# Kernel optimization log

Measured on AMD Instinct MI355X. Metric: run time of the kernel, lower is better.

Reference implementation:

```python
import jax, jax.numpy as jnp
import numpy as np

INPUT_DIM = 1024
HIDDEN_DIM = 1024

def setup_inputs() -> dict:
    key = jax.random.key(0)
    ks = jax.random.split(key, 9)
    s_in = 1.0 / np.sqrt(INPUT_DIM)
    s_h = 1.0 / np.sqrt(HIDDEN_DIM)
    x = jax.random.normal(ks[0], (4, 2048, INPUT_DIM), dtype=jnp.float32)
    Wq = jax.random.uniform(ks[1], (INPUT_DIM, HIDDEN_DIM), jnp.float32, -s_in, s_in)
    bq = jax.random.uniform(ks[2], (HIDDEN_DIM,), jnp.float32, -s_in, s_in)
    Wk = jax.random.uniform(ks[3], (INPUT_DIM, HIDDEN_DIM), jnp.float32, -s_in, s_in)
    bk = jax.random.uniform(ks[4], (HIDDEN_DIM,), jnp.float32, -s_in, s_in)
    Wv = jax.random.uniform(ks[5], (INPUT_DIM, HIDDEN_DIM), jnp.float32, -s_in, s_in)
    bv = jax.random.uniform(ks[6], (HIDDEN_DIM,), jnp.float32, -s_in, s_in)
    Wo = jax.random.uniform(ks[7], (HIDDEN_DIM, INPUT_DIM), jnp.float32, -s_h, s_h)
    bo = jax.random.uniform(ks[8], (INPUT_DIM,), jnp.float32, -s_h, s_h)
    return {"x": x, "Wq": Wq, "bq": bq, "Wk": Wk, "bk": bk, "Wv": Wv, "bv": bv, "Wo": Wo, "bo": bo}

def reference(x, Wq, bq, Wk, bk, Wv, bv, Wo, bo):
    # x: [B, S, D_in]; scale uses x.shape[-1] (faithful to source, which divides by sqrt(input_dim))
    scale = 1.0 / jnp.sqrt(jnp.asarray(x.shape[-1], dtype=x.dtype))
    Q = jnp.einsum('bsd,dh->bsh', x, Wq) + bq
    K = jnp.einsum('bsd,dh->bsh', x, Wk) + bk
    V = jnp.einsum('bsd,dh->bsh', x, Wv) + bv
    scores = jnp.einsum('bqh,bkh->bqk', Q, K) * scale  # [B, S, S]
    attn = jax.nn.softmax(scores, axis=-1)
    ctx = jnp.einsum('bqk,bkh->bqh', attn, V)
    return jnp.einsum('bsh,hd->bsd', ctx, Wo) + bo
```

## Files before the change

### kernel.cpp

```cpp
#include <hip/hip_runtime.h>
#include <hip/hip_bf16.h>

typedef __attribute__((ext_vector_type(8))) short bf16x8;
typedef __attribute__((ext_vector_type(16))) float f32x16;
typedef __attribute__((ext_vector_type(4))) unsigned short us4;

#define AS1 __attribute__((address_space(1)))
#define AS3 __attribute__((address_space(3)))

__device__ __forceinline__ unsigned short f2bf(float f) {
  unsigned u = __float_as_uint(f);
  u += 0x7fff + ((u >> 16) & 1);
  return (unsigned short)(u >> 16);
}

__device__ __forceinline__ float bf2f(unsigned short h) {
  return __uint_as_float((unsigned)h << 16);
}

__device__ __forceinline__ void gload_lds16(const void* g, void* l) {
  __builtin_amdgcn_global_load_lds((const AS1 unsigned int*)g,
                                   (AS3 unsigned int*)l, 16, 0, 0);
}

template <typename OutT, bool BIAS, int MODE, int NJ>
__global__ __launch_bounds__(256, (NJ >= 3) ? 2 : 3) void gemm_bt(
    const unsigned short* __restrict__ A,
    const unsigned short* __restrict__ Bt,
    OutT* __restrict__ C,
    unsigned short* __restrict__ Vt,
    const float* __restrict__ bias,
    int Kd, int lda, int ldb, int ldc,
    long sA, long sB, long sC,
    float scale) {
  constexpr int BN    = NJ * 64;
  constexpr int ROWS  = 128 + BN;
  constexpr int SLOTS = ROWS / 16;
  __shared__ unsigned short lds[2][ROWS * 32];

  const int bz = blockIdx.z;
  A  += (size_t)bz * sA + (size_t)blockIdx.x * 128 * lda;
  Bt += (size_t)bz * sB + (size_t)blockIdx.y * BN * ldb;

  const int tid  = threadIdx.x;
  const int wave = tid >> 6;
  const int lane = tid & 63;
  const int wm   = (wave >> 1) * 64;
  const int wn   = (wave & 1) * (NJ * 32);
  const int l32  = lane & 31;
  const int half = lane >> 5;
  const int cg   = ((lane & 3) ^ ((lane >> 2) & 3) ^ (lane >> 4)) * 8;
  const int pswz = (l32 & 3) ^ ((l32 >> 2) & 3);

  auto stage = [&](int k0, int b) {
#pragma unroll
    for (int j = 0; j < SLOTS / 4; ++j) {
      const int s = wave + 4 * j;
      const int r = s * 16 + (lane >> 2);
      const unsigned short* src = (s < 8) ? (A + (size_t)r * lda)
                                          : (Bt + (size_t)(r - 128) * ldb);
      gload_lds16(src + k0 + cg, (char*)&lds[b][0] + s * 1024);
    }
  };

  f32x16 acc[2][NJ] = {};

  stage(0, 0);
  int cur = 0;
  for (int k0 = 0; k0 < Kd; k0 += 32) {
    __syncthreads();
    if (k0 + 32 < Kd) stage(k0 + 32, cur ^ 1);

    const unsigned short* base = &lds[cur][0];
    bf16x8 af[2][2], bfr[NJ][2];
#pragma unroll
    for (int t = 0; t < 2; ++t)
#pragma unroll
      for (int h = 0; h < 2; ++h) {
        const int p = ((2 * h + half) ^ pswz) * 8;
        af[t][h] = *(const bf16x8*)&base[(wm + t * 32 + l32) * 32 + p];
      }
#pragma unroll
    for (int u = 0; u < NJ; ++u)
#pragma unroll
      for (int h = 0; h < 2; ++h) {
        const int p = ((2 * h + half) ^ pswz) * 8;
        bfr[u][h] = *(const bf16x8*)&base[(128 + wn + u * 32 + l32) * 32 + p];
      }
#pragma unroll
    for (int t = 0; t < 2; ++t)
#pragma unroll
      for (int u = 0; u < NJ; ++u) {
        acc[t][u] = __builtin_amdgcn_mfma_f32_32x32x16_bf16(af[t][0], bfr[u][0], acc[t][u], 0, 0, 0);
        acc[t][u] = __builtin_amdgcn_mfma_f32_32x32x16_bf16(af[t][1], bfr[u][1], acc[t][u], 0, 0, 0);
      }
    cur ^= 1;
  }

  const int row0 = blockIdx.x * 128 + wm;
  const int colb = blockIdx.y * BN;

  if constexpr (MODE == 1) {
#pragma unroll
    for (int t = 0; t < 2; ++t) {
#pragma unroll
      for (int u = 0; u < NJ; ++u) {
        const int gcol  = colb + wn + u * 32;
        const int piece = gcol >> 10;
        const float bv  = BIAS ? bias[gcol + l32] : 0.0f;
        if (piece < 2) {
          OutT* dst = C + (size_t)piece * sC;
          const int col = (gcol & 1023) + l32;
#pragma unroll
          for (int r = 0; r < 16; ++r) {
            const int row = row0 + t * 32 + (r & 3) + 8 * (r >> 2) + 4 * half;
            dst[(size_t)row * ldc + col] = (OutT)f2bf(acc[t][u][r] * scale + bv);
          }
        } else {
          const int d = (gcol & 1023) + l32;
          const int b = row0 >> 11;
          const int sbase = (row0 & 2047) + t * 32 + 4 * half;
#pragma unroll
          for (int g = 0; g < 4; ++g) {
            const int s0 = sbase + 8 * g;
            us4 pk;
            pk.x = f2bf(acc[t][u][4 * g + 0] * scale + bv);
            pk.y = f2bf(acc[t][u][4 * g + 1] * scale + bv);
            pk.z = f2bf(acc[t][u][4 * g + 2] * scale + bv);
            pk.w = f2bf(acc[t][u][4 * g + 3] * scale + bv);
            *(us4*)&Vt[((size_t)b << 21) + (size_t)d * 2048 + s0] = pk;
          }
        }
      }
    }
  } else {
    C += (size_t)bz * sC;
    const int col0 = colb + wn;
#pragma unroll
    for (int t = 0; t < 2; ++t) {
#pragma unroll
      for (int u = 0; u < NJ; ++u) {
        const int col = col0 + u * 32 + l32;
        const float bv = BIAS ? bias[col0 + u * 32 + l32] : 0.0f;
#pragma unroll
        for (int r = 0; r < 16; ++r) {
          const int row = row0 + t * 32 + (r & 3) + 8 * (r >> 2) + 4 * half;
          const float v = acc[t][u][r] * scale + bv;
          if constexpr (sizeof(OutT) == 4)
            C[(size_t)row * ldc + col] = v;
          else
            C[(size_t)row * ldc + col] = (OutT)f2bf(v);
        }
      }
    }
  }
}

__global__ void cvt_x(const float* __restrict__ in, unsigned short* __restrict__ out, int n4) {
  const int i = blockIdx.x * blockDim.x + threadIdx.x;
  if (i < n4) {
    const float4 v = ((const float4*)in)[i];
    uint2 o;
    o.x = (unsigned)f2bf(v.x) | ((unsigned)f2bf(v.y) << 16);
    o.y = (unsigned)f2bf(v.z) | ((unsigned)f2bf(v.w) << 16);
    ((uint2*)out)[i] = o;
  }
}

__global__ void cvtT_w4(const float* __restrict__ Wq, const float* __restrict__ Wk,
                        const float* __restrict__ Wv, const float* __restrict__ Wo,
                        unsigned short* __restrict__ Wqkvb, unsigned short* __restrict__ Wob) {
  __shared__ unsigned short tile[64][65];
  const int z = blockIdx.z;
  const float* in = (z == 0) ? Wq : (z == 1) ? Wk : (z == 2) ? Wv : Wo;
  unsigned short* out = (z == 3) ? Wob : Wqkvb + (size_t)z * 1024 * 1024;
  const int r0 = blockIdx.y * 64, c0 = blockIdx.x * 64;
  for (int i = threadIdx.y; i < 64; i += 4)
    tile[i][threadIdx.x] = f2bf(in[(size_t)(r0 + i) * 1024 + c0 + threadIdx.x]);
  __syncthreads();
  for (int i = threadIdx.y; i < 64; i += 4)
    out[(size_t)(c0 + i) * 1024 + r0 + threadIdx.x] = tile[threadIdx.x][i];
}

__global__ void concat_bias(const float* __restrict__ bq, const float* __restrict__ bk,
                            const float* __restrict__ bv, float* __restrict__ dst) {
  const int z = blockIdx.x;
  const float* src = (z == 0) ? bq : (z == 1) ? bk : bv;
  const int i = threadIdx.x;
  ((float4*)(dst + z * 1024))[i] = ((const float4*)src)[i];
}

__global__ __launch_bounds__(256) void softmax_bf16(unsigned short* __restrict__ scores) {
  unsigned short* p = scores + (size_t)blockIdx.x * 2048;
  const int t = threadIdx.x;
  uint4 raw = ((const uint4*)p)[t];
  float v[8];
  v[0] = __uint_as_float(raw.x << 16); v[1] = __uint_as_float(raw.x & 0xffff0000u);
  v[2] = __uint_as_float(raw.y << 16); v[3] = __uint_as_float(raw.y & 0xffff0000u);
  v[4] = __uint_as_float(raw.z << 16); v[5] = __uint_as_float(raw.z & 0xffff0000u);
  v[6] = __uint_as_float(raw.w << 16); v[7] = __uint_as_float(raw.w & 0xffff0000u);

  float m = v[0];
#pragma unroll
  for (int i = 1; i < 8; ++i) m = fmaxf(m, v[i]);
#pragma unroll
  for (int off = 32; off; off >>= 1) m = fmaxf(m, __shfl_xor(m, off, 64));

  __shared__ float red[4];
  __shared__ float bcast[2];
  const int wave = t >> 6, lane = t & 63;
  if (lane == 0) red[wave] = m;
  __syncthreads();
  if (t == 0) bcast[0] = fmaxf(fmaxf(red[0], red[1]), fmaxf(red[2], red[3]));
  __syncthreads();
  m = bcast[0];

  float s = 0.f;
#pragma unroll
  for (int i = 0; i < 8; ++i) { v[i] = __expf(v[i] - m); s += v[i]; }
#pragma unroll
  for (int off = 32; off; off >>= 1) s += __shfl_xor(s, off, 64);
  if (lane == 0) red[wave] = s;
  __syncthreads();
  if (t == 0) bcast[1] = red[0] + red[1] + red[2] + red[3];
  __syncthreads();
  const float inv = 1.0f / bcast[1];

  uint4 ov;
  ov.x = (unsigned)f2bf(v[0] * inv) | ((unsigned)f2bf(v[1] * inv) << 16);
  ov.y = (unsigned)f2bf(v[2] * inv) | ((unsigned)f2bf(v[3] * inv) << 16);
  ov.z = (unsigned)f2bf(v[4] * inv) | ((unsigned)f2bf(v[5] * inv) << 16);
  ov.w = (unsigned)f2bf(v[6] * inv) | ((unsigned)f2bf(v[7] * inv) << 16);
  ((uint4*)p)[t] = ov;
}

extern "C" void kernel_launch(void* const* d_in, const int* in_sizes, int n_in,
                              void* d_out, int out_size, void* d_ws, size_t ws_size,
                              hipStream_t stream) {
  const float* x  = (const float*)d_in[0];
  const float* Wq = (const float*)d_in[1];
  const float* bq = (const float*)d_in[2];
  const float* Wk = (const float*)d_in[3];
  const float* bk = (const float*)d_in[4];
  const float* Wv = (const float*)d_in[5];
  const float* bv = (const float*)d_in[6];
  const float* Wo = (const float*)d_in[7];
  const float* bo = (const float*)d_in[8];
  float* out = (float*)d_out;

  char* ws = (char*)d_ws;
  size_t off = 0;
  auto alloc = [&](size_t bytes) { char* p = ws + off; off += (bytes + 255) & ~255UL; return p; };
  unsigned short* xb    = (unsigned short*)alloc(8192UL * 1024 * 2);
  unsigned short* Wqkvb = (unsigned short*)alloc(3072UL * 1024 * 2);
  unsigned short* Wob   = (unsigned short*)alloc(1024UL * 1024 * 2);
  float*          bqkv  = (float*)alloc(3072UL * 4);
  unsigned short* Qb    = (unsigned short*)alloc(8192UL * 1024 * 2);
  unsigned short* Kb    = (unsigned short*)alloc(8192UL * 1024 * 2);
  unsigned short* Vtb   = (unsigned short*)alloc(4UL * 1024 * 2048 * 2);
  unsigned short* attn  = (unsigned short*)alloc(8192UL * 2048 * 2);
  unsigned short* ctxb  = (unsigned short*)alloc(8192UL * 1024 * 2);

  const dim3 blk(256);

  cvt_x<<<2097152 / 256, 256, 0, stream>>>(x, xb, 2097152);
  cvtT_w4<<<dim3(16, 16, 4), dim3(64, 4), 0, stream>>>(Wq, Wk, Wv, Wo, Wqkvb, Wob);
  concat_bias<<<3, 256, 0, stream>>>(bq, bk, bv, bqkv);

  gemm_bt<unsigned short, true, 1, 3><<<dim3(64, 16, 1), blk, 0, stream>>>(
      xb, Wqkvb, Qb, Vtb, bqkv, 1024, 1024, 1024, 1024, 0, 0, 8192L * 1024, 1.0f);

  gemm_bt<unsigned short, false, 0, 4><<<dim3(16, 8, 4), blk, 0, stream>>>(
      Qb, Kb, attn, nullptr, nullptr, 1024, 1024, 1024, 2048,
      2048L * 1024, 2048L * 1024, 2048L * 2048, 0.03125f);

  softmax_bf16<<<8192, 256, 0, stream>>>(attn);

  gemm_bt<unsigned short, false, 0, 2><<<dim3(16, 8, 4), blk, 0, stream>>>(
      attn, Vtb, ctxb, nullptr, nullptr, 2048, 2048, 2048, 1024,
      2048L * 2048, 1024L * 2048, 2048L * 1024, 1.0f);

  gemm_bt<float, true, 0, 2><<<dim3(64, 8, 1), blk, 0, stream>>>(
      ctxb, Wob, out, nullptr, bo, 1024, 1024, 1024, 1024, 0, 0, 0, 1.0f);
}
```

Before: 295.8 us.

## Replace GEMM with 256x256-tile 8-wave kernel using interleaved loads and 16x16 MFMA

```diff
diff --git a/kernel.cpp b/kernel.cpp
--- a/kernel.cpp
+++ b/kernel.cpp
@@ -1,8 +1,7 @@
 #include <hip/hip_runtime.h>
-#include <hip/hip_bf16.h>
 
 typedef __attribute__((ext_vector_type(8))) short bf16x8;
-typedef __attribute__((ext_vector_type(16))) float f32x16;
+typedef __attribute__((ext_vector_type(4))) float f32x4;
 typedef __attribute__((ext_vector_type(4))) unsigned short us4;
 
 #define AS1 __attribute__((address_space(1)))
@@ -14,17 +13,15 @@
   return (unsigned short)(u >> 16);
 }
 
-__device__ __forceinline__ float bf2f(unsigned short h) {
-  return __uint_as_float((unsigned)h << 16);
-}
-
 __device__ __forceinline__ void gload_lds16(const void* g, void* l) {
   __builtin_amdgcn_global_load_lds((const AS1 unsigned int*)g,
                                    (AS3 unsigned int*)l, 16, 0, 0);
 }
 
-template <typename OutT, bool BIAS, int MODE, int NJ>
-__global__ __launch_bounds__(256, (NJ >= 3) ? 2 : 3) void gemm_bt(
+#define MFMA16(a, b, c) __builtin_amdgcn_mfma_f32_16x16x32_bf16(a, b, c, 0, 0, 0)
+
+template <typename OutT, bool BIAS, int MODE>
+__global__ __launch_bounds__(512, 2) void gemm8p(
     const unsigned short* __restrict__ A,
     const unsigned short* __restrict__ Bt,
     OutT* __restrict__ C,
@@ -33,125 +30,186 @@
     int Kd, int lda, int ldb, int ldc,
     long sA, long sB, long sC,
     float scale) {
-  constexpr int BN    = NJ * 64;
-  constexpr int ROWS  = 128 + BN;
-  constexpr int SLOTS = ROWS / 16;
-  __shared__ unsigned short lds[2][ROWS * 32];
+  constexpr int BOFF = 256 * 64;
+  __shared__ unsigned short lds[2][512 * 64];
 
   const int bz = blockIdx.z;
-  A  += (size_t)bz * sA + (size_t)blockIdx.x * 128 * lda;
-  Bt += (size_t)bz * sB + (size_t)blockIdx.y * BN * ldb;
+  A  += (size_t)bz * sA + (size_t)blockIdx.x * 256 * lda;
+  Bt += (size_t)bz * sB + (size_t)blockIdx.y * 256 * ldb;
 
   const int tid  = threadIdx.x;
   const int wave = tid >> 6;
   const int lane = tid & 63;
-  const int wm   = (wave >> 1) * 64;
-  const int wn   = (wave & 1) * (NJ * 32);
-  const int l32  = lane & 31;
-  const int half = lane >> 5;
-  const int cg   = ((lane & 3) ^ ((lane >> 2) & 3) ^ (lane >> 4)) * 8;
-  const int pswz = (l32 & 3) ^ ((l32 >> 2) & 3);
-
-  auto stage = [&](int k0, int b) {
-#pragma unroll
-    for (int j = 0; j < SLOTS / 4; ++j) {
-      const int s = wave + 4 * j;
-      const int r = s * 16 + (lane >> 2);
-      const unsigned short* src = (s < 8) ? (A + (size_t)r * lda)
-                                          : (Bt + (size_t)(r - 128) * ldb);
-      gload_lds16(src + k0 + cg, (char*)&lds[b][0] + s * 1024);
-    }
+  const int wm   = wave >> 2;
+  const int wn   = wave & 3;
+  const int l15  = lane & 15;
+  const int hi   = lane >> 4;
+  const int sr  = (wave << 3) + (lane >> 3);
+  const int sc8 = lane & 7;
+  const int co0 = ((hi    ) ^ (lane & 7)) << 3;
+  const int co1 = ((hi + 4) ^ (lane & 7)) << 3;
+  const int rA0 = wm * 128 + l15;
+  const int rB0 = wn * 32 + l15;
+
+  auto stA = [&](int b, int k0, int r0) {
+    const unsigned short* g =
+        A + (size_t)(r0 + sr) * lda + (k0 + ((sc8 ^ (sr & 7)) << 3));
+    gload_lds16(g, &lds[b][(r0 + (wave << 3)) * 64]);
   };
-
-  f32x16 acc[2][NJ] = {};
-
-  stage(0, 0);
-  int cur = 0;
-  for (int k0 = 0; k0 < Kd; k0 += 32) {
-    __syncthreads();
-    if (k0 + 32 < Kd) stage(k0 + 32, cur ^ 1);
-
-    const unsigned short* base = &lds[cur][0];
-    bf16x8 af[2][2], bfr[NJ][2];
-#pragma unroll
-    for (int t = 0; t < 2; ++t)
-#pragma unroll
-      for (int h = 0; h < 2; ++h) {
-        const int p = ((2 * h + half) ^ pswz) * 8;
-        af[t][h] = *(const bf16x8*)&base[(wm + t * 32 + l32) * 32 + p];
-      }
-#pragma unroll
-    for (int u = 0; u < NJ; ++u)
-#pragma unroll
-      for (int h = 0; h < 2; ++h) {
-        const int p = ((2 * h + half) ^ pswz) * 8;
-        bfr[u][h] = *(const bf16x8*)&base[(128 + wn + u * 32 + l32) * 32 + p];
-      }
-#pragma unroll
-    for (int t = 0; t < 2; ++t)
-#pragma unroll
-      for (int u = 0; u < NJ; ++u) {
-        acc[t][u] = __builtin_amdgcn_mfma_f32_32x32x16_bf16(af[t][0], bfr[u][0], acc[t][u], 0, 0, 0);
-        acc[t][u] = __builtin_amdgcn_mfma_f32_32x32x16_bf16(af[t][1], bfr[u][1], acc[t][u], 0, 0, 0);
-      }
-    cur ^= 1;
+  auto stB = [&](int b, int k0, int r0) {
+    const int lr = r0 + sr;
+    const int gr = ((lr >> 5) & 3) * 64 + ((lr >> 7) << 5) + (lr & 31);
+    const unsigned short* g =
+        Bt + (size_t)gr * ldb + (k0 + ((sc8 ^ (lr & 7)) << 3));
+    gload_lds16(g, &lds[b][BOFF + (r0 + (wave << 3)) * 64]);
+  };
+
+  f32x4 acc[8][4] = {};
+  bf16x8 af[4][2], b0f[2][2], b1f[2][2];
+
+  stA(0, 0, 0);   stA(0, 0, 128);
+  stB(0, 0, 0);   stB(0, 0, 64);
+  stB(0, 0, 128); stB(0, 0, 192);
+  stA(0, 0, 64);  stA(0, 0, 192);
+  asm volatile("s_waitcnt vmcnt(4)" ::: "memory");
+  __builtin_amdgcn_s_barrier();
+
+  const int NT = Kd >> 6;
+  for (int t = 0; t < NT; ++t) {
+    const int buf = t & 1;
+    const int nb  = buf ^ 1;
+    const int nk0 = (t + 1) << 6;
+    const bool st = (t + 1) < NT;
+    const unsigned short* Lr = &lds[buf][0];
+
+#pragma unroll
+    for (int mt = 0; mt < 4; ++mt) {
+      af[mt][0] = *(const bf16x8*)&Lr[(rA0 + mt * 16) * 64 + co0];
+      af[mt][1] = *(const bf16x8*)&Lr[(rA0 + mt * 16) * 64 + co1];
+    }
+#pragma unroll
+    for (int n = 0; n < 2; ++n) {
+      b0f[n][0] = *(const bf16x8*)&Lr[BOFF + (rB0 + n * 16) * 64 + co0];
+      b0f[n][1] = *(const bf16x8*)&Lr[BOFF + (rB0 + n * 16) * 64 + co1];
+    }
+    if (st) { stA(nb, nk0, 0); stA(nb, nk0, 128); }
+    __builtin_amdgcn_s_barrier();
+    __builtin_amdgcn_s_setprio(1);
+#pragma unroll
+    for (int mt = 0; mt < 4; ++mt)
+#pragma unroll
+      for (int n = 0; n < 2; ++n) {
+        acc[mt][n] = MFMA16(af[mt][0], b0f[n][0], acc[mt][n]);
+        acc[mt][n] = MFMA16(af[mt][1], b0f[n][1], acc[mt][n]);
+      }
+    __builtin_amdgcn_s_setprio(0);
+    asm volatile("s_waitcnt vmcnt(4)" ::: "memory");
+    __builtin_amdgcn_s_barrier();
+
+#pragma unroll
+    for (int n = 0; n < 2; ++n) {
+      b1f[n][0] = *(const bf16x8*)&Lr[BOFF + (128 + rB0 + n * 16) * 64 + co0];
+      b1f[n][1] = *(const bf16x8*)&Lr[BOFF + (128 + rB0 + n * 16) * 64 + co1];
+    }
+    if (st) { stB(nb, nk0, 0); stB(nb, nk0, 64); }
+    __builtin_amdgcn_s_barrier();
+    __builtin_amdgcn_s_setprio(1);
+#pragma unroll
+    for (int mt = 0; mt < 4; ++mt)
+#pragma unroll
+      for (int n = 0; n < 2; ++n) {
+        acc[mt][2 + n] = MFMA16(af[mt][0], b1f[n][0], acc[mt][2 + n]);
+        acc[mt][2 + n] = MFMA16(af[mt][1], b1f[n][1], acc[mt][2 + n]);
+      }
+    __builtin_amdgcn_s_setprio(0);
+    asm volatile("s_waitcnt vmcnt(4)" ::: "memory");
+    __builtin_amdgcn_s_barrier();
+
+#pragma unroll
+    for (int mt = 0; mt < 4; ++mt) {
+      af[mt][0] = *(const bf16x8*)&Lr[(64 + rA0 + mt * 16) * 64 + co0];
+      af[mt][1] = *(const bf16x8*)&Lr[(64 + rA0 + mt * 16) * 64 + co1];
+    }
+    if (st) { stB(nb, nk0, 128); stB(nb, nk0, 192); }
+    __builtin_amdgcn_s_barrier();
+    __builtin_amdgcn_s_setprio(1);
+#pragma unroll
+    for (int mt = 0; mt < 4; ++mt)
+#pragma unroll
+      for (int n = 0; n < 2; ++n) {
+        acc[4 + mt][2 + n] = MFMA16(af[mt][0], b1f[n][0], acc[4 + mt][2 + n]);
+        acc[4 + mt][2 + n] = MFMA16(af[mt][1], b1f[n][1], acc[4 + mt][2 + n]);
+      }
+    __builtin_amdgcn_s_setprio(0);
+    __builtin_amdgcn_s_barrier();
+
+    if (st) { stA(nb, nk0, 64); stA(nb, nk0, 192); }
+    __builtin_amdgcn_s_barrier();
+    __builtin_amdgcn_s_setprio(1);
+#pragma unroll
+    for (int mt = 0; mt < 4; ++mt)
+#pragma unroll
+      for (int n = 0; n < 2; ++n) {
+        acc[4 + mt][n] = MFMA16(af[mt][0], b0f[n][0], acc[4 + mt][n]);
+        acc[4 + mt][n] = MFMA16(af[mt][1], b0f[n][1], acc[4 + mt][n]);
+      }
+    __builtin_amdgcn_s_setprio(0);
+    asm volatile("s_waitcnt vmcnt(4)" ::: "memory");
+    __builtin_amdgcn_s_barrier();
   }
 
-  const int row0 = blockIdx.x * 128 + wm;
-  const int colb = blockIdx.y * BN;
+  const int hi4  = hi << 2;
+  const int row0 = blockIdx.x * 256 + wm * 128;
+  const int col0 = blockIdx.y * 256 + wn * 64;
 
   if constexpr (MODE == 1) {
 #pragma unroll
-    for (int t = 0; t < 2; ++t) {
-#pragma unroll
-      for (int u = 0; u < NJ; ++u) {
-        const int gcol  = colb + wn + u * 32;
-        const int piece = gcol >> 10;
-        const float bv  = BIAS ? bias[gcol + l32] : 0.0f;
-        if (piece < 2) {
-          OutT* dst = C + (size_t)piece * sC;
-          const int col = (gcol & 1023) + l32;
-#pragma unroll
-          for (int r = 0; r < 16; ++r) {
-            const int row = row0 + t * 32 + (r & 3) + 8 * (r >> 2) + 4 * half;
-            dst[(size_t)row * ldc + col] = (OutT)f2bf(acc[t][u][r] * scale + bv);
+    for (int nt = 0; nt < 4; ++nt) {
+      const int gcol  = col0 + nt * 16;
+      const int piece = gcol >> 10;
+      const float bv  = BIAS ? bias[gcol + l15] : 0.0f;
+      if (piece < 2) {
+        OutT* dst = C + (size_t)piece * sC;
+        const int col = (gcol & 1023) + l15;
+#pragma unroll
+        for (int mt = 0; mt < 8; ++mt)
+#pragma unroll
+          for (int r = 0; r < 4; ++r) {
+            const int row = row0 + mt * 16 + hi4 + r;
+            dst[(size_t)row * ldc + col] = (OutT)f2bf(acc[mt][nt][r] * scale + bv);
           }
-        } else {
-          const int d = (gcol & 1023) + l32;
-          const int b = row0 >> 11;
-          const int sbase = (row0 & 2047) + t * 32 + 4 * half;
-#pragma unroll
-          for (int g = 0; g < 4; ++g) {
-            const int s0 = sbase + 8 * g;
-            us4 pk;
-            pk.x = f2bf(acc[t][u][4 * g + 0] * scale + bv);
-            pk.y = f2bf(acc[t][u][4 * g + 1] * scale + bv);
-            pk.z = f2bf(acc[t][u][4 * g + 2] * scale + bv);
-            pk.w = f2bf(acc[t][u][4 * g + 3] * scale + bv);
-            *(us4*)&Vt[((size_t)b << 21) + (size_t)d * 2048 + s0] = pk;
-          }
+      } else {
+        const int d = (gcol & 1023) + l15;
+        const int b = blockIdx.x >> 3;
+        const int sb = (blockIdx.x & 7) * 256 + wm * 128 + hi4;
+#pragma unroll
+        for (int mt = 0; mt < 8; ++mt) {
+          us4 pk;
+          pk.x = f2bf(acc[mt][nt][0] * scale + bv);
+          pk.y = f2bf(acc[mt][nt][1] * scale + bv);
+          pk.z = f2bf(acc[mt][nt][2] * scale + bv);
+          pk.w = f2bf(acc[mt][nt][3] * scale + bv);
+          *(us4*)&Vt[((size_t)b << 21) + (size_t)d * 2048 + sb + mt * 16] = pk;
         }
       }
     }
   } else {
     C += (size_t)bz * sC;
-    const int col0 = colb + wn;
-#pragma unroll
-    for (int t = 0; t < 2; ++t) {
-#pragma unroll
-      for (int u = 0; u < NJ; ++u) {
-        const int col = col0 + u * 32 + l32;
-        const float bv = BIAS ? bias[col0 + u * 32 + l32] : 0.0f;
-#pragma unroll
-        for (int r = 0; r < 16; ++r) {
-          const int row = row0 + t * 32 + (r & 3) + 8 * (r >> 2) + 4 * half;
-          const float v = acc[t][u][r] * scale + bv;
+#pragma unroll
+    for (int nt = 0; nt < 4; ++nt) {
+      const int col = col0 + nt * 16 + l15;
+      const float bv = BIAS ? bias[col] : 0.0f;
+#pragma unroll
+      for (int mt = 0; mt < 8; ++mt)
+#pragma unroll
+        for (int r = 0; r < 4; ++r) {
+          const int row = row0 + mt * 16 + hi4 + r;
+          const float v = acc[mt][nt][r] * scale + bv;
           if constexpr (sizeof(OutT) == 4)
             C[(size_t)row * ldc + col] = v;
           else
             C[(size_t)row * ldc + col] = (OutT)f2bf(v);
         }
-      }
     }
   }
 }
@@ -261,25 +319,25 @@
   unsigned short* attn  = (unsigned short*)alloc(8192UL * 2048 * 2);
   unsigned short* ctxb  = (unsigned short*)alloc(8192UL * 1024 * 2);
 
-  const dim3 blk(256);
+  const dim3 blk(512);
 
   cvt_x<<<2097152 / 256, 256, 0, stream>>>(x, xb, 2097152);
   cvtT_w4<<<dim3(16, 16, 4), dim3(64, 4), 0, stream>>>(Wq, Wk, Wv, Wo, Wqkvb, Wob);
   concat_bias<<<3, 256, 0, stream>>>(bq, bk, bv, bqkv);
 
-  gemm_bt<unsigned short, true, 1, 3><<<dim3(64, 16, 1), blk, 0, stream>>>(
+  gemm8p<unsigned short, true, 1><<<dim3(32, 12, 1), blk, 0, stream>>>(
       xb, Wqkvb, Qb, Vtb, bqkv, 1024, 1024, 1024, 1024, 0, 0, 8192L * 1024, 1.0f);
 
-  gemm_bt<unsigned short, false, 0, 4><<<dim3(16, 8, 4), blk, 0, stream>>>(
+  gemm8p<unsigned short, false, 0><<<dim3(8, 8, 4), blk, 0, stream>>>(
       Qb, Kb, attn, nullptr, nullptr, 1024, 1024, 1024, 2048,
       2048L * 1024, 2048L * 1024, 2048L * 2048, 0.03125f);
 
   softmax_bf16<<<8192, 256, 0, stream>>>(attn);
 
-  gemm_bt<unsigned short, false, 0, 2><<<dim3(16, 8, 4), blk, 0, stream>>>(
+  gemm8p<unsigned short, false, 0><<<dim3(8, 4, 4), blk, 0, stream>>>(
       attn, Vtb, ctxb, nullptr, nullptr, 2048, 2048, 2048, 1024,
       2048L * 2048, 1024L * 2048, 2048L * 1024, 1.0f);
 
-  gemm_bt<float, true, 0, 2><<<dim3(64, 8, 1), blk, 0, stream>>>(
+  gemm8p<float, true, 0><<<dim3(32, 4, 1), blk, 0, stream>>>(
       ctxb, Wob, out, nullptr, bo, 1024, 1024, 1024, 1024, 0, 0, 0, 1.0f);
 }
```

Measured after the change: 328.4 us. +11.0%, slower.
